# Kernel optimization log

Measured on AMD Instinct MI355X. Metric: run time of the kernel, lower is better.

The kernel has to match this reference:

```python
import jax, jax.numpy as jnp
import numpy as np

BN_EPS = 1e-5  # torch BatchNorm1d default


def setup_inputs() -> dict:
    key = jax.random.key(0)
    k = jax.random.split(key, 5)
    B, D, L = 4096, 4096, 4  # batch, width, num layers (3 hidden + 1 output)
    x = jax.random.normal(k[0], (B, D), dtype=jnp.float32)
    # Per-layer Linear weights stored as [L, in, out]; scaled like xavier-ish init.
    W = jax.random.normal(k[1], (L, D, D), dtype=jnp.float32) * (1.0 / np.sqrt(D))
    b = jax.random.normal(k[2], (L, D), dtype=jnp.float32) * 0.01
    gamma = jax.random.uniform(k[3], (L, D), dtype=jnp.float32, minval=0.5, maxval=1.5)
    beta = jax.random.normal(k[4], (L, D), dtype=jnp.float32) * 0.1
    return {"x": x, "W": W, "b": b, "gamma": gamma, "beta": beta}


def _layer(h, W_l, b_l, gamma_l, beta_l):
    # one big GEMM replaces the per-neuron GEMV loop + stack
    h = h @ W_l + b_l  # [B, out]
    # BatchNorm1d, training mode: biased batch stats over the batch dim
    mu = jnp.mean(h, axis=0)
    var = jnp.var(h, axis=0)
    h = (h - mu) * jax.lax.rsqrt(var + BN_EPS) * gamma_l + beta_l
    return jax.nn.relu(h)


def reference(x, W, b, gamma, beta):
    out = x
    for l in range(W.shape[0]):  # small fixed layer count
        out = _layer(out, W[l], b[l], gamma[l], beta[l])
    # nn.Softmax(dim=0): softmax over the batch dimension, as in the original
    return jax.nn.softmax(out, axis=0)
```

## Files before the change

### kernel.cpp

```cpp
#include <hip/hip_runtime.h>
#include <stdint.h>

#define DIMD 4096
#define DIMB 4096
#define NLAYER 4
#define NT (DIMD / 64)

typedef unsigned short u16;
typedef __attribute__((ext_vector_type(4))) float f32x4;
typedef __attribute__((ext_vector_type(8))) __bf16 bf16x8;

__device__ __forceinline__ u16 f2bf(float f) {
    union { float f; uint32_t u; } v; v.f = f;
    return (u16)((v.u + 0x7fffu + ((v.u >> 16) & 1u)) >> 16);
}
__device__ __forceinline__ float bf2f(u16 u) {
    union { uint32_t u; float f; } v; v.u = ((uint32_t)u) << 16;
    return v.f;
}

__global__ void k_cvt(const float* __restrict__ in, u16* __restrict__ out) {
    int i = (blockIdx.x * 256 + threadIdx.x) * 4;
    float4 v = *reinterpret_cast<const float4*>(in + i);
    ushort4 r;
    r.x = f2bf(v.x); r.y = f2bf(v.y); r.z = f2bf(v.z); r.w = f2bf(v.w);
    *reinterpret_cast<ushort4*>(out + i) = r;
}

__global__ void k_trans(const float* __restrict__ W, u16* __restrict__ Wt) {
    __shared__ float tile[64][65];
    const int t = threadIdx.x;
    const size_t loff = (size_t)blockIdx.z * DIMD * DIMD;
    const int n0 = blockIdx.x * 64, k0 = blockIdx.y * 64;
    const int kr = t >> 4, c4 = (t & 15) * 4;
    #pragma unroll
    for (int r = 0; r < 4; ++r) {
        float4 v = *reinterpret_cast<const float4*>(W + loff + (size_t)(k0 + kr + r * 16) * DIMD + n0 + c4);
        tile[kr + r * 16][c4 + 0] = v.x;
        tile[kr + r * 16][c4 + 1] = v.y;
        tile[kr + r * 16][c4 + 2] = v.z;
        tile[kr + r * 16][c4 + 3] = v.w;
    }
    __syncthreads();
    const int nr = t >> 4, k4 = (t & 15) * 4;
    #pragma unroll
    for (int r = 0; r < 4; ++r) {
        int n = nr + r * 16;
        ushort4 o;
        o.x = f2bf(tile[k4 + 0][n]);
        o.y = f2bf(tile[k4 + 1][n]);
        o.z = f2bf(tile[k4 + 2][n]);
        o.w = f2bf(tile[k4 + 3][n]);
        *reinterpret_cast<ushort4*>(Wt + loff + (size_t)(n0 + n) * DIMD + k0 + k4) = o;
    }
}

#define GLD(g, l) __builtin_amdgcn_global_load_lds( \
    (__attribute__((address_space(1))) void*)(g),   \
    (__attribute__((address_space(3))) void*)(l), 16, 0, 0)

__global__ __launch_bounds__(512, 2) void k_gemm(
        const u16* __restrict__ A, const u16* __restrict__ Bt,
        const float* __restrict__ bias, u16* __restrict__ H,
        float* __restrict__ Hf,
        float* __restrict__ csum, float* __restrict__ csum2) {
    __shared__ __attribute__((aligned(16))) u16 As[2 * 256 * 64];
    __shared__ __attribute__((aligned(16))) u16 Bs[2 * 256 * 64];
    const int tid = threadIdx.x;
    const int lane = tid & 63, wv = tid >> 6;
    const int wm = wv >> 2, wn = wv & 3;
    const int bm = blockIdx.y, bn = blockIdx.x;
    const int lr = lane & 15, lk = lane >> 4;

    const int r0 = tid >> 3;
    const int cswz = (tid & 7) ^ (r0 & 7);
    const u16* gA = A  + (size_t)(bm * 256 + r0) * DIMD + cswz * 8;
    const u16* gB = Bt + (size_t)(bn * 256 + r0) * DIMD + cswz * 8;

#define STAGE_A(h, t, buf) do { \
    const u16* _s = gA + (size_t)(h) * 128 * DIMD + (size_t)(t) * 64; \
    u16* _d = As + (buf) * 16384 + (h) * 8192 + wv * 512; \
    GLD(_s, _d); GLD(_s + (size_t)64 * DIMD, _d + 4096); \
} while (0)
#define STAGE_B(h, t, buf) do { \
    const u16* _s = gB + (size_t)(h) * 128 * DIMD + (size_t)(t) * 64; \
    u16* _d = Bs + (buf) * 16384 + (h) * 8192 + wv * 512; \
    GLD(_s, _d); GLD(_s + (size_t)64 * DIMD, _d + 4096); \
} while (0)

    int aoff[4][2], boff[4][2];
    #pragma unroll
    for (int mf = 0; mf < 4; ++mf)
        #pragma unroll
        for (int ks = 0; ks < 2; ++ks) {
            int row = wm * 128 + mf * 16 + lr;
            aoff[mf][ks] = row * 64 + ((ks * 4 + lk) ^ (row & 7)) * 8;
        }
    #pragma unroll
    for (int nf = 0; nf < 4; ++nf)
        #pragma unroll
        for (int ks = 0; ks < 2; ++ks) {
            int row = wn * 64 + nf * 16 + lr;
            boff[nf][ks] = row * 64 + ((ks * 4 + lk) ^ (row & 7)) * 8;
        }

    f32x4 acc[8][4] = {};
    bf16x8 aS0[4], aS1[4], bk0[4], bk1[4];

    STAGE_B(0, 0, 0); STAGE_B(1, 0, 0);
    STAGE_B(0, 1, 1); STAGE_B(1, 1, 1);
    STAGE_A(0, 0, 0); STAGE_A(1, 0, 0);
    asm volatile("s_waitcnt vmcnt(0)" ::: "memory");
    __builtin_amdgcn_s_barrier();

    for (int t = 0; t < NT; ++t) {
        const int cur = t & 1;
        const u16* Ab = As + cur * 16384;
        const u16* Bb = Bs + cur * 16384;

        if (t + 1 < NT) { STAGE_A(0, t + 1, cur ^ 1); STAGE_A(1, t + 1, cur ^ 1); }
        #pragma unroll
        for (int mf = 0; mf < 4; ++mf)
            aS0[mf] = *reinterpret_cast<const bf16x8*>(Ab + aoff[mf][0]);
        #pragma unroll
        for (int nf = 0; nf < 4; ++nf)
            bk0[nf] = *reinterpret_cast<const bf16x8*>(Bb + boff[nf][0]);
        #pragma unroll
        for (int mf = 0; mf < 4; ++mf)
            aS1[mf] = *reinterpret_cast<const bf16x8*>(Ab + 4096 + aoff[mf][0]);
        asm volatile("s_waitcnt lgkmcnt(4)" ::: "memory");
        __builtin_amdgcn_sched_barrier(0);
        __builtin_amdgcn_s_setprio(1);
        #pragma unroll
        for (int mf = 0; mf < 4; ++mf)
            #pragma unroll
            for (int nf = 0; nf < 4; ++nf)
                acc[mf][nf] = __builtin_amdgcn_mfma_f32_16x16x32_bf16(
                    aS0[mf], bk0[nf], acc[mf][nf], 0, 0, 0);
        __builtin_amdgcn_s_setprio(0);
        __builtin_amdgcn_s_barrier();

        #pragma unroll
        for (int mf = 0; mf < 4; ++mf)
            aS0[mf] = *reinterpret_cast<const bf16x8*>(Ab + 4096 + aoff[mf][1]);
        #pragma unroll
        for (int nf = 0; nf < 4; ++nf)
            bk1[nf] = *reinterpret_cast<const bf16x8*>(Bb + boff[nf][1]);
        asm volatile("s_waitcnt lgkmcnt(8)" ::: "memory");
        __builtin_amdgcn_sched_barrier(0);
        __builtin_amdgcn_s_setprio(1);
        #pragma unroll
        for (int mf = 0; mf < 4; ++mf)
            #pragma unroll
            for (int nf = 0; nf < 4; ++nf)
                acc[4 + mf][nf] = __builtin_amdgcn_mfma_f32_16x16x32_bf16(
                    aS1[mf], bk0[nf], acc[4 + mf][nf], 0, 0, 0);
        __builtin_amdgcn_s_setprio(0);
        __builtin_amdgcn_s_barrier();

        #pragma unroll
        for (int mf = 0; mf < 4; ++mf)
            aS1[mf] = *reinterpret_cast<const bf16x8*>(Ab + aoff[mf][1]);
        asm volatile("s_waitcnt lgkmcnt(4)" ::: "memory");
        __builtin_amdgcn_sched_barrier(0);
        __builtin_amdgcn_s_setprio(1);
        #pragma unroll
        for (int mf = 0; mf < 4; ++mf)
            #pragma unroll
            for (int nf = 0; nf < 4; ++nf)
                acc[4 + mf][nf] = __builtin_amdgcn_mfma_f32_16x16x32_bf16(
                    aS0[mf], bk1[nf], acc[4 + mf][nf], 0, 0, 0);
        __builtin_amdgcn_s_setprio(0);
        __builtin_amdgcn_s_barrier();

        if (t + 2 < NT) { STAGE_B(0, t + 2, cur); STAGE_B(1, t + 2, cur); }
        asm volatile("s_waitcnt lgkmcnt(0)" ::: "memory");
        __builtin_amdgcn_sched_barrier(0);
        __builtin_amdgcn_s_setprio(1);
        #pragma unroll
        for (int mf = 0; mf < 4; ++mf)
            #pragma unroll
            for (int nf = 0; nf < 4; ++nf)
                acc[mf][nf] = __builtin_amdgcn_mfma_f32_16x16x32_bf16(
                    aS1[mf], bk1[nf], acc[mf][nf], 0, 0, 0);
        __builtin_amdgcn_s_setprio(0);
        if (t + 2 < NT) asm volatile("s_waitcnt vmcnt(4)" ::: "memory");
        else            asm volatile("s_waitcnt vmcnt(0)" ::: "memory");
        __builtin_amdgcn_s_barrier();
    }

    #pragma unroll
    for (int nf = 0; nf < 4; ++nf) {
        int col = bn * 256 + wn * 64 + nf * 16 + lr;
        float bv = bias[col];
        float s1 = 0.f, s2 = 0.f;
        #pragma unroll
        for (int m = 0; m < 8; ++m) {
            int rbase = bm * 256 + wm * 128 + (m >> 2) * 64 + (m & 3) * 16 + lk * 4;
            #pragma unroll
            for (int r = 0; r < 4; ++r) {
                float v = acc[m][nf][r] + bv;
                if (Hf) Hf[(size_t)(rbase + r) * DIMD + col] = v;
                else    H [(size_t)(rbase + r) * DIMD + col] = f2bf(v);
                s1 += v; s2 += v * v;
            }
        }
        s1 += __shfl_xor(s1, 16); s1 += __shfl_xor(s1, 32);
        s2 += __shfl_xor(s2, 16); s2 += __shfl_xor(s2, 32);
        if (lk == 0) {
            atomicAdd(&csum[col], s1);
            atomicAdd(&csum2[col], s2);
        }
    }
#undef STAGE_A
#undef STAGE_B
}

__global__ void k_norm(const u16* __restrict__ H, const float* __restrict__ sum,
                       const float* __restrict__ sum2, const float* __restrict__ gamma,
                       const float* __restrict__ beta, u16* __restrict__ o) {
    int j = (blockIdx.x * 256 + threadIdx.x) * 4;
    int i0 = blockIdx.y * 32;
    float4 sm = *reinterpret_cast<const float4*>(sum + j);
    float4 s2 = *reinterpret_cast<const float4*>(sum2 + j);
    float4 gm = *reinterpret_cast<const float4*>(gamma + j);
    float4 bt = *reinterpret_cast<const float4*>(beta + j);
    float s[4], tt[4];
    #pragma unroll
    for (int c = 0; c < 4; ++c) {
        float mu = (&sm.x)[c] * (1.0f / DIMB);
        float var = (&s2.x)[c] * (1.0f / DIMB) - mu * mu;
        s[c] = (&gm.x)[c] * rsqrtf(var + 1e-5f);
        tt[c] = (&bt.x)[c] - mu * s[c];
    }
    for (int i = i0; i < i0 + 32; ++i) {
        ushort4 h = *reinterpret_cast<const ushort4*>(H + (size_t)i * DIMD + j);
        ushort4 r;
        #pragma unroll
        for (int c = 0; c < 4; ++c)
            (&r.x)[c] = f2bf(fmaxf(bf2f((&h.x)[c]) * s[c] + tt[c], 0.0f));
        *reinterpret_cast<ushort4*>(o + (size_t)i * DIMD + j) = r;
    }
}

__global__ void k_esum(const float* __restrict__ H, const float* __restrict__ sum,
                       const float* __restrict__ sum2, const float* __restrict__ gamma,
                       const float* __restrict__ beta, float* __restrict__ esum) {
    int j = (blockIdx.x * 256 + threadIdx.x) * 4;
    int i0 = blockIdx.y * 32;
    float4 sm = *reinterpret_cast<const float4*>(sum + j);
    float4 s2 = *reinterpret_cast<const float4*>(sum2 + j);
    float4 gm = *reinterpret_cast<const float4*>(gamma + j);
    float4 bt = *reinterpret_cast<const float4*>(beta + j);
    float s[4], tt[4], acc[4] = {0.f, 0.f, 0.f, 0.f};
    #pragma unroll
    for (int c = 0; c < 4; ++c) {
        float mu = (&sm.x)[c] * (1.0f / DIMB);
        float var = (&s2.x)[c] * (1.0f / DIMB) - mu * mu;
        s[c] = (&gm.x)[c] * rsqrtf(var + 1e-5f);
        tt[c] = (&bt.x)[c] - mu * s[c];
    }
    for (int i = i0; i < i0 + 32; ++i) {
        float4 h = *reinterpret_cast<const float4*>(H + (size_t)i * DIMD + j);
        #pragma unroll
        for (int c = 0; c < 4; ++c)
            acc[c] += __expf(fmaxf((&h.x)[c] * s[c] + tt[c], 0.0f));
    }
    #pragma unroll
    for (int c = 0; c < 4; ++c) atomicAdd(&esum[j + c], acc[c]);
}

__global__ void k_final(float* __restrict__ H, const float* __restrict__ sum,
                        const float* __restrict__ sum2, const float* __restrict__ gamma,
                        const float* __restrict__ beta, const float* __restrict__ esum) {
    int j = (blockIdx.x * 256 + threadIdx.x) * 4;
    int i0 = blockIdx.y * 32;
    float4 sm = *reinterpret_cast<const float4*>(sum + j);
    float4 s2 = *reinterpret_cast<const float4*>(sum2 + j);
    float4 gm = *reinterpret_cast<const float4*>(gamma + j);
    float4 bt = *reinterpret_cast<const float4*>(beta + j);
    float4 es = *reinterpret_cast<const float4*>(esum + j);
    float s[4], tt[4], inv[4];
    #pragma unroll
    for (int c = 0; c < 4; ++c) {
        float mu = (&sm.x)[c] * (1.0f / DIMB);
        float var = (&s2.x)[c] * (1.0f / DIMB) - mu * mu;
        s[c] = (&gm.x)[c] * rsqrtf(var + 1e-5f);
        tt[c] = (&bt.x)[c] - mu * s[c];
        inv[c] = 1.0f / (&es.x)[c];
    }
    for (int i = i0; i < i0 + 32; ++i) {
        float4 h = *reinterpret_cast<const float4*>(H + (size_t)i * DIMD + j);
        float4 o;
        #pragma unroll
        for (int c = 0; c < 4; ++c)
            (&o.x)[c] = __expf(fmaxf((&h.x)[c] * s[c] + tt[c], 0.0f)) * inv[c];
        *reinterpret_cast<float4*>(H + (size_t)i * DIMD + j) = o;
    }
}

extern "C" void kernel_launch(void* const* d_in, const int* in_sizes, int n_in,
                              void* d_out, int out_size, void* d_ws, size_t ws_size,
                              hipStream_t stream) {
    (void)in_sizes; (void)n_in; (void)out_size; (void)ws_size;
    const float* x     = (const float*)d_in[0];
    const float* W     = (const float*)d_in[1];
    const float* b     = (const float*)d_in[2];
    const float* gamma = (const float*)d_in[3];
    const float* beta  = (const float*)d_in[4];
    float* out = (float*)d_out;

    char* ws = (char*)d_ws;
    u16*  Abf = (u16*)ws;
    u16*  Wt4 = (u16*)(ws + (size_t)32 * 1024 * 1024);
    u16*  Hbf = (u16*)(ws + (size_t)160 * 1024 * 1024);
    float* stats = (float*)(ws + (size_t)192 * 1024 * 1024);
    hipMemsetAsync(stats, 0, (4 * 8192 + 4096) * sizeof(float), stream);

    k_cvt<<<DIMB * DIMD / 1024, 256, 0, stream>>>(x, Abf);
    k_trans<<<dim3(64, 64, 4), 256, 0, stream>>>(W, Wt4);

    for (int l = 0; l < NLAYER; ++l) {
        float* sum = stats + l * 8192;
        float* sum2 = sum + 4096;
        float* Hf = (l == NLAYER - 1) ? out : nullptr;
        k_gemm<<<dim3(16, 16), 512, 0, stream>>>(Abf, Wt4 + (size_t)l * DIMD * DIMD,
                                                 b + l * DIMD, Hbf, Hf, sum, sum2);
        if (l < NLAYER - 1)
            k_norm<<<dim3(4, 128), 256, 0, stream>>>(Hbf, sum, sum2,
                gamma + l * DIMD, beta + l * DIMD, Abf);
    }
    k_esum<<<dim3(4, 128), 256, 0, stream>>>(out, stats + 3 * 8192, stats + 3 * 8192 + 4096,
        gamma + 3 * DIMD, beta + 3 * DIMD, stats + 32768);
    k_final<<<dim3(4, 128), 256, 0, stream>>>(out, stats + 3 * 8192, stats + 3 * 8192 + 4096,
        gamma + 3 * DIMD, beta + 3 * DIMD, stats + 32768);
}
```

Measured before the change: 785.7 us.

## Restructure GEMM main loop into quadrant MFMA phases with deeper prefetch

Rewrites the bf16 GEMM inner loop so each K-tile is processed as four quadrant phases (A-lo/A-hi by B-half), each phase doing both k-substeps. The loop is unrolled by two over the double buffers. A and B loads for tile t+2 are issued into the current buffer partway through the tile, and waits use vmcnt(8). The epilogue is remapped so accumulator columns match the new B half layout. The aim is better overlap of global-to-LDS loads with MFMA work and fewer LDS reads per MFMA. The cost is more barriers per tile and a riskier buffer-reuse ordering, since the current buffer is overwritten while it is still being read.

Result: faster. 708.0 us (-9.9%).

```diff
diff --git a/kernel.cpp b/kernel.cpp
--- a/kernel.cpp
+++ b/kernel.cpp
@@ -58,6 +58,10 @@
 #define GLD(g, l) __builtin_amdgcn_global_load_lds( \
     (__attribute__((address_space(1))) void*)(g),   \
     (__attribute__((address_space(3))) void*)(l), 16, 0, 0)
+
+#define VMW8 asm volatile("s_waitcnt vmcnt(8)" ::: "memory")
+#define VMW0 asm volatile("s_waitcnt vmcnt(0)" ::: "memory")
+#define LGKM0 asm volatile("s_waitcnt lgkmcnt(0)" ::: "memory")
 
 __global__ __launch_bounds__(512, 2) void k_gemm(
         const u16* __restrict__ A, const u16* __restrict__ Bt,
@@ -88,7 +92,7 @@
     GLD(_s, _d); GLD(_s + (size_t)64 * DIMD, _d + 4096); \
 } while (0)
 
-    int aoff[4][2], boff[4][2];
+    int aoff[4][2], boff[2][2];
     #pragma unroll
     for (int mf = 0; mf < 4; ++mf)
         #pragma unroll
@@ -97,7 +101,7 @@
             aoff[mf][ks] = row * 64 + ((ks * 4 + lk) ^ (row & 7)) * 8;
         }
     #pragma unroll
-    for (int nf = 0; nf < 4; ++nf)
+    for (int nf = 0; nf < 2; ++nf)
         #pragma unroll
         for (int ks = 0; ks < 2; ++ks) {
             int row = wn * 64 + nf * 16 + lr;
@@ -105,113 +109,102 @@
         }
 
     f32x4 acc[8][4] = {};
-    bf16x8 aS0[4], aS1[4], bk0[4], bk1[4];
-
-    STAGE_B(0, 0, 0); STAGE_B(1, 0, 0);
-    STAGE_B(0, 1, 1); STAGE_B(1, 1, 1);
-    STAGE_A(0, 0, 0); STAGE_A(1, 0, 0);
-    asm volatile("s_waitcnt vmcnt(0)" ::: "memory");
+    bf16x8 a[4][2], b0[2][2], b1[2][2];
+
+#define READ_ALO(Ab) _Pragma("unroll") for (int mf = 0; mf < 4; ++mf) \
+    _Pragma("unroll") for (int ks = 0; ks < 2; ++ks) \
+        a[mf][ks] = *reinterpret_cast<const bf16x8*>((Ab) + aoff[mf][ks])
+#define READ_AHI(Ab) _Pragma("unroll") for (int mf = 0; mf < 4; ++mf) \
+    _Pragma("unroll") for (int ks = 0; ks < 2; ++ks) \
+        a[mf][ks] = *reinterpret_cast<const bf16x8*>((Ab) + 4096 + aoff[mf][ks])
+#define READ_B0(Bb) _Pragma("unroll") for (int nf = 0; nf < 2; ++nf) \
+    _Pragma("unroll") for (int ks = 0; ks < 2; ++ks) \
+        b0[nf][ks] = *reinterpret_cast<const bf16x8*>((Bb) + boff[nf][ks])
+#define READ_B1(Bb) _Pragma("unroll") for (int nf = 0; nf < 2; ++nf) \
+    _Pragma("unroll") for (int ks = 0; ks < 2; ++ks) \
+        b1[nf][ks] = *reinterpret_cast<const bf16x8*>((Bb) + 2048 + boff[nf][ks])
+#define MFMA_Q(MO, B, NO) _Pragma("unroll") for (int mf = 0; mf < 4; ++mf) \
+    _Pragma("unroll") for (int nf = 0; nf < 2; ++nf) \
+    _Pragma("unroll") for (int ks = 0; ks < 2; ++ks) \
+        acc[(MO) + mf][(NO) + nf] = __builtin_amdgcn_mfma_f32_16x16x32_bf16( \
+            a[mf][ks], B[nf][ks], acc[(MO) + mf][(NO) + nf], 0, 0, 0)
+
+#define TILE(CUR, TN, PF, WEND) do { \
+    const u16* Ab = As + (CUR) * 16384; \
+    const u16* Bb = Bs + (CUR) * 16384; \
+     \
+    READ_ALO(Ab); READ_B0(Bb); \
+    __builtin_amdgcn_s_barrier(); \
+    LGKM0; \
+    __builtin_amdgcn_s_setprio(1); \
+    MFMA_Q(0, b0, 0); \
+    __builtin_amdgcn_s_setprio(0); \
+    __builtin_amdgcn_s_barrier(); \
+     \
+    READ_B1(Bb); \
+    __builtin_amdgcn_s_barrier(); \
+    LGKM0; \
+    __builtin_amdgcn_s_setprio(1); \
+    MFMA_Q(0, b1, 2); \
+    __builtin_amdgcn_s_setprio(0); \
+    __builtin_amdgcn_s_barrier(); \
+     \
+    READ_AHI(Ab); \
+    if (PF) { STAGE_B(0, TN, CUR); STAGE_B(1, TN, CUR); } \
+    __builtin_amdgcn_s_barrier(); \
+    LGKM0; \
+    __builtin_amdgcn_s_setprio(1); \
+    MFMA_Q(4, b1, 2); \
+    __builtin_amdgcn_s_setprio(0); \
+    __builtin_amdgcn_s_barrier(); \
+     \
+    if (PF) { STAGE_A(0, TN, CUR); STAGE_A(1, TN, CUR); } \
+    __builtin_amdgcn_s_setprio(1); \
+    MFMA_Q(4, b0, 0); \
+    __builtin_amdgcn_s_setprio(0); \
+    WEND; \
+    __builtin_amdgcn_s_barrier(); \
+} while (0)
+
+    STAGE_B(0, 0, 0); STAGE_B(1, 0, 0); STAGE_A(0, 0, 0); STAGE_A(1, 0, 0);
+    STAGE_B(0, 1, 1); STAGE_B(1, 1, 1); STAGE_A(0, 1, 1); STAGE_A(1, 1, 1);
+    VMW8;
     __builtin_amdgcn_s_barrier();
 
-    for (int t = 0; t < NT; ++t) {
-        const int cur = t & 1;
-        const u16* Ab = As + cur * 16384;
-        const u16* Bb = Bs + cur * 16384;
-
-        if (t + 1 < NT) { STAGE_A(0, t + 1, cur ^ 1); STAGE_A(1, t + 1, cur ^ 1); }
-        #pragma unroll
-        for (int mf = 0; mf < 4; ++mf)
-            aS0[mf] = *reinterpret_cast<const bf16x8*>(Ab + aoff[mf][0]);
-        #pragma unroll
-        for (int nf = 0; nf < 4; ++nf)
-            bk0[nf] = *reinterpret_cast<const bf16x8*>(Bb + boff[nf][0]);
-        #pragma unroll
-        for (int mf = 0; mf < 4; ++mf)
-            aS1[mf] = *reinterpret_cast<const bf16x8*>(Ab + 4096 + aoff[mf][0]);
-        asm volatile("s_waitcnt lgkmcnt(4)" ::: "memory");
-        __builtin_amdgcn_sched_barrier(0);
-        __builtin_amdgcn_s_setprio(1);
-        #pragma unroll
-        for (int mf = 0; mf < 4; ++mf)
+    for (int tt = 0; tt < NT - 2; tt += 2) {
+        TILE(0, tt + 2, true, VMW8);
+        TILE(1, tt + 3, true, VMW8);
+    }
+    TILE(0, 0, false, VMW0);
+    TILE(1, 0, false, VMW0);
+
+    #pragma unroll
+    for (int nh = 0; nh < 2; ++nh)
+        #pragma unroll
+        for (int nf = 0; nf < 2; ++nf) {
+            int n = nh * 2 + nf;
+            int col = bn * 256 + wn * 64 + nh * 32 + nf * 16 + lr;
+            float bv = bias[col];
+            float s1 = 0.f, s2 = 0.f;
             #pragma unroll
-            for (int nf = 0; nf < 4; ++nf)
-                acc[mf][nf] = __builtin_amdgcn_mfma_f32_16x16x32_bf16(
-                    aS0[mf], bk0[nf], acc[mf][nf], 0, 0, 0);
-        __builtin_amdgcn_s_setprio(0);
-        __builtin_amdgcn_s_barrier();
-
-        #pragma unroll
-        for (int mf = 0; mf < 4; ++mf)
-            aS0[mf] = *reinterpret_cast<const bf16x8*>(Ab + 4096 + aoff[mf][1]);
-        #pragma unroll
-        for (int nf = 0; nf < 4; ++nf)
-            bk1[nf] = *reinterpret_cast<const bf16x8*>(Bb + boff[nf][1]);
-        asm volatile("s_waitcnt lgkmcnt(8)" ::: "memory");
-        __builtin_amdgcn_sched_barrier(0);
-        __builtin_amdgcn_s_setprio(1);
-        #pragma unroll
-        for (int mf = 0; mf < 4; ++mf)
-            #pragma unroll
-            for (int nf = 0; nf < 4; ++nf)
-                acc[4 + mf][nf] = __builtin_amdgcn_mfma_f32_16x16x32_bf16(
-                    aS1[mf], bk0[nf], acc[4 + mf][nf], 0, 0, 0);
-        __builtin_amdgcn_s_setprio(0);
-        __builtin_amdgcn_s_barrier();
-
-        #pragma unroll
-        for (int mf = 0; mf < 4; ++mf)
-            aS1[mf] = *reinterpret_cast<const bf16x8*>(Ab + aoff[mf][1]);
-        asm volatile("s_waitcnt lgkmcnt(4)" ::: "memory");
-        __builtin_amdgcn_sched_barrier(0);
-        __builtin_amdgcn_s_setprio(1);
-        #pragma unroll
-        for (int mf = 0; mf < 4; ++mf)
-            #pragma unroll
-            for (int nf = 0; nf < 4; ++nf)
-                acc[4 + mf][nf] = __builtin_amdgcn_mfma_f32_16x16x32_bf16(
-                    aS0[mf], bk1[nf], acc[4 + mf][nf], 0, 0, 0);
-        __builtin_amdgcn_s_setprio(0);
-        __builtin_amdgcn_s_barrier();
-
-        if (t + 2 < NT) { STAGE_B(0, t + 2, cur); STAGE_B(1, t + 2, cur); }
-        asm volatile("s_waitcnt lgkmcnt(0)" ::: "memory");
-        __builtin_amdgcn_sched_barrier(0);
-        __builtin_amdgcn_s_setprio(1);
-        #pragma unroll
-        for (int mf = 0; mf < 4; ++mf)
-            #pragma unroll
-            for (int nf = 0; nf < 4; ++nf)
-                acc[mf][nf] = __builtin_amdgcn_mfma_f32_16x16x32_bf16(
-                    aS1[mf], bk1[nf], acc[mf][nf], 0, 0, 0);
-        __builtin_amdgcn_s_setprio(0);
-        if (t + 2 < NT) asm volatile("s_waitcnt vmcnt(4)" ::: "memory");
-        else            asm volatile("s_waitcnt vmcnt(0)" ::: "memory");
-        __builtin_amdgcn_s_barrier();
-    }
-
-    #pragma unroll
-    for (int nf = 0; nf < 4; ++nf) {
-        int col = bn * 256 + wn * 64 + nf * 16 + lr;
-        float bv = bias[col];
-        float s1 = 0.f, s2 = 0.f;
-        #pragma unroll
-        for (int m = 0; m < 8; ++m) {
-            int rbase = bm * 256 + wm * 128 + (m >> 2) * 64 + (m & 3) * 16 + lk * 4;
-            #pragma unroll
-            for (int r = 0; r < 4; ++r) {
-                float v = acc[m][nf][r] + bv;
-                if (Hf) Hf[(size_t)(rbase + r) * DIMD + col] = v;
-                else    H [(size_t)(rbase + r) * DIMD + col] = f2bf(v);
-                s1 += v; s2 += v * v;
+            for (int m = 0; m < 8; ++m) {
+                int rbase = bm * 256 + wm * 128 + (m >> 2) * 64 + (m & 3) * 16 + lk * 4;
+                #pragma unroll
+                for (int r = 0; r < 4; ++r) {
+                    float v = acc[m][n][r] + bv;
+                    if (Hf) Hf[(size_t)(rbase + r) * DIMD + col] = v;
+                    else    H [(size_t)(rbase + r) * DIMD + col] = f2bf(v);
+                    s1 += v; s2 += v * v;
+                }
+            }
+            s1 += __shfl_xor(s1, 16); s1 += __shfl_xor(s1, 32);
+            s2 += __shfl_xor(s2, 16); s2 += __shfl_xor(s2, 32);
+            if (lk == 0) {
+                atomicAdd(&csum[col], s1);
+                atomicAdd(&csum2[col], s2);
             }
         }
-        s1 += __shfl_xor(s1, 16); s1 += __shfl_xor(s1, 32);
-        s2 += __shfl_xor(s2, 16); s2 += __shfl_xor(s2, 32);
-        if (lk == 0) {
-            atomicAdd(&csum[col], s1);
-            atomicAdd(&csum2[col], s2);
-        }
-    }
+#undef TILE
 #undef STAGE_A
 #undef STAGE_B
 }
```
